# Optimization experiments

Hardware: AMD Instinct MI355X
Metric: run time of the kernel (lower is better)

## Reference

```python
import jax, jax.numpy as jnp
import numpy as np

HIDDEN = 2048
N_HEADS = 16
N_KV_HEADS = 4
HEAD_DIM = HIDDEN // N_HEADS  # 128
N_GROUPS = N_HEADS // N_KV_HEADS  # 4


def rotate_half(x):
    # interleaved rotate: (-x_odd, x_even) interleaved back
    x_even = x[..., ::2]
    x_odd = x[..., 1::2]
    return jnp.stack((-x_odd, x_even), axis=-1).reshape(x.shape)


def setup_inputs() -> dict:
    key = jax.random.key(0)
    ks = jax.random.split(key, 8)
    B, S = 4, 2048
    x = jax.random.normal(ks[0], (B, S, HIDDEN), dtype=jnp.float32)
    # RoPE tables (precomputed cos/sin over max positions)
    inv_freq = 1.0 / (1000000.0 ** (np.arange(0, HEAD_DIM, 2, dtype=np.float32) / HEAD_DIM))
    t = np.arange(S, dtype=np.float32)
    freqs = np.outer(t, inv_freq)  # [S, HEAD_DIM/2]
    emb = np.repeat(freqs, 2, axis=-1)  # interleaved layout [S, HEAD_DIM]
    cos = jnp.asarray(np.cos(emb))
    sin = jnp.asarray(np.sin(emb))
    scale = 0.02
    Wq = jax.random.normal(ks[1], (HIDDEN, N_HEADS * HEAD_DIM), dtype=jnp.float32) * scale
    Wk = jax.random.normal(ks[2], (HIDDEN, N_KV_HEADS * HEAD_DIM), dtype=jnp.float32) * scale
    Wv = jax.random.normal(ks[3], (HIDDEN, N_KV_HEADS * HEAD_DIM), dtype=jnp.float32) * scale
    Wo = jax.random.normal(ks[4], (N_HEADS * HEAD_DIM, HIDDEN), dtype=jnp.float32) * scale
    return {"x": x, "cos": cos, "sin": sin, "Wq": Wq, "Wk": Wk, "Wv": Wv, "Wo": Wo}


def reference(x, cos, sin, Wq, Wk, Wv, Wo):
    B, S, D = x.shape
    q = (x @ Wq).reshape(B, S, N_HEADS, HEAD_DIM).transpose(0, 2, 1, 3)      # [B,H,S,d]
    k = (x @ Wk).reshape(B, S, N_KV_HEADS, HEAD_DIM).transpose(0, 2, 1, 3)   # [B,Hkv,S,d]
    v = (x @ Wv).reshape(B, S, N_KV_HEADS, HEAD_DIM).transpose(0, 2, 1, 3)
    # RoPE: position_ids = arange(S); cos/sin [S,d] -> [1,1,S,d]
    c = cos[:S][None, None, :, :]
    s = sin[:S][None, None, :, :]
    q = q * c + rotate_half(q) * s
    k = k * c + rotate_half(k) * s
    # repeat_kv: [B,Hkv,S,d] -> [B,H,S,d]
    k = jnp.repeat(k, N_GROUPS, axis=1)
    v = jnp.repeat(v, N_GROUPS, axis=1)
    # causal SDPA
    scores = jnp.einsum("bhqd,bhkd->bhqk", q, k) / jnp.sqrt(jnp.float32(HEAD_DIM))
    neg = jnp.finfo(scores.dtype).min
    causal = jnp.triu(jnp.full((S, S), neg, dtype=scores.dtype), k=1)
    scores = scores + causal[None, None]
    attn = jax.nn.softmax(scores.astype(jnp.float32), axis=-1).astype(q.dtype)
    out = jnp.einsum("bhqk,bhkd->bhqd", attn, v)
    out = out.transpose(0, 2, 1, 3).reshape(B, S, N_HEADS * HEAD_DIM)
    return out @ Wo
```

## Files before the change

kernel.cpp:

```cpp
#include <hip/hip_runtime.h>
#include <stdint.h>

#define S_LEN 2048
#define BATCH 4
#define HID   2048
#define HD    128
#define NKV   4
#define MTOT  (BATCH*S_LEN)
#define NQT2  (S_LEN/256)
#define QSCALE 0.08838834764831845f

typedef float    f32x4  __attribute__((ext_vector_type(4)));
typedef __bf16   bf16x8 __attribute__((ext_vector_type(8)));
typedef __bf16   bf16x4 __attribute__((ext_vector_type(4)));
typedef unsigned u32x2  __attribute__((ext_vector_type(2)));

__device__ __forceinline__ void gld16(const void* g, void* l) {
    __builtin_amdgcn_global_load_lds(
        (const __attribute__((address_space(1))) void*)g,
        (__attribute__((address_space(3))) void*)l, 16, 0, 0);
}

__global__ void k_conv_x(const float* __restrict__ in, __bf16* __restrict__ out) {
    int i = blockIdx.x * blockDim.x + threadIdx.x;
    f32x4 a = ((const f32x4*)in)[2 * i];
    f32x4 b = ((const f32x4*)in)[2 * i + 1];
    bf16x8 o;
    o[0] = (__bf16)a[0]; o[1] = (__bf16)a[1]; o[2] = (__bf16)a[2]; o[3] = (__bf16)a[3];
    o[4] = (__bf16)b[0]; o[5] = (__bf16)b[1]; o[6] = (__bf16)b[2]; o[7] = (__bf16)b[3];
    ((bf16x8*)out)[i] = o;
}

__global__ void k_transpose_all(const float* __restrict__ Wq,
                                const float* __restrict__ Wk,
                                const float* __restrict__ Wv,
                                const float* __restrict__ Wo,
                                __bf16* __restrict__ wqt,
                                __bf16* __restrict__ wkvt,
                                __bf16* __restrict__ wot) {
    const int z = blockIdx.z;
    const float* in; __bf16* out; int N;
    if      (z == 0) { in = Wq; out = wqt;  N = 2048; }
    else if (z == 1) { in = Wk; out = wkvt; N = 512;  }
    else if (z == 2) { in = Wv; out = wkvt + (size_t)512 * HID; N = 512; }
    else             { in = Wo; out = wot;  N = 2048; }
    int k0 = blockIdx.x * 64, n0 = blockIdx.y * 64;
    if (n0 >= N) return;
    __shared__ float tile[64][65];
    for (int e = threadIdx.x; e < 4096; e += 256) {
        int r = e >> 6, c = e & 63;
        tile[r][c] = in[(size_t)(k0 + r) * N + n0 + c];
    }
    __syncthreads();
    for (int e = threadIdx.x; e < 4096; e += 256) {
        int r = e >> 6, c = e & 63;
        out[(size_t)(n0 + r) * HID + k0 + c] = (__bf16)tile[c][r];
    }
}

#define BARM asm volatile("s_barrier" ::: "memory")
#define BAR1 do { BARM;                                                       \
                  asm volatile("s_waitcnt lgkmcnt(0)" ::: "memory");          \
                  __builtin_amdgcn_sched_barrier(0); } while (0)
#define BAR2 BARM
#define MM(qm, qn)                                                            \
    do {                                                                      \
        __builtin_amdgcn_s_setprio(1);                                        \
        _Pragma("unroll") for (int ks = 0; ks < 2; ks++)                      \
        _Pragma("unroll") for (int mf = 0; mf < 4; mf++)                      \
        _Pragma("unroll") for (int nf = 0; nf < 2; nf++)                      \
            acc[qm][qn][mf][nf] = __builtin_amdgcn_mfma_f32_16x16x32_bf16(    \
                af[mf][ks], bf[nf][ks], acc[qm][qn][mf][nf], 0, 0, 0);        \
        __builtin_amdgcn_s_setprio(0);                                        \
    } while (0)

#define GEMM8_BODY(Aptr, Bptr)                                                \
    __shared__ __bf16 Ab[2][2][128 * 64];                                     \
    __shared__ __bf16 Bb[2][2][128 * 64];                                     \
    const int tid = threadIdx.x, lane = tid & 63, wave = tid >> 6;            \
    const int wm = wave >> 2, wn = wave & 3;                                  \
    const int lo = lane & 15, hi = lane >> 4;                                 \
    f32x4 acc[2][2][4][2] = {};                                               \
    const int srow = wave * 8 + (lane >> 3);                                  \
    const int sp   = lane & 7;                                                \
    auto STA = [&](int s, int h, int t) {                                     \
        _Pragma("unroll") for (int p = 0; p < 2; p++) {                       \
            int rr = p * 64 + srow;                                           \
            int c = sp ^ (rr & 7);                                            \
            gld16(Aptr + (size_t)(m0 + h * 128 + rr) * HID + t * 64 + c * 8,  \
                  &Ab[s][h][(p * 64 + wave * 8) * 64]);                       \
        }                                                                     \
    };                                                                        \
    auto STB = [&](int s, int h, int t) {                                     \
        _Pragma("unroll") for (int p = 0; p < 2; p++) {                       \
            int rr = p * 64 + srow;                                           \
            int c = sp ^ (rr & 7);                                            \
            gld16(Bptr + (size_t)(n0 + h * 128 + rr) * HID + t * 64 + c * 8,  \
                  &Bb[s][h][(p * 64 + wave * 8) * 64]);                       \
        }                                                                     \
    };                                                                        \
    bf16x8 af[4][2], bf[2][2];                                                \
    auto LDA = [&](int s, int qm) {                                           \
        _Pragma("unroll") for (int mf = 0; mf < 4; mf++) {                    \
            int rr = wm * 64 + mf * 16 + lo;                                  \
            _Pragma("unroll") for (int ks = 0; ks < 2; ks++) {                \
                int pp = (ks * 4 + hi) ^ (rr & 7);                            \
                af[mf][ks] = *(const bf16x8*)&Ab[s][qm][rr * 64 + pp * 8];    \
            }                                                                 \
        }                                                                     \
    };                                                                        \
    auto LDB = [&](int s, int qn) {                                           \
        _Pragma("unroll") for (int nf = 0; nf < 2; nf++) {                    \
            int rr = wn * 32 + nf * 16 + lo;                                  \
            _Pragma("unroll") for (int ks = 0; ks < 2; ks++) {                \
                int pp = (ks * 4 + hi) ^ (rr & 7);                            \
                bf[nf][ks] = *(const bf16x8*)&Bb[s][qn][rr * 64 + pp * 8];    \
            }                                                                 \
        }                                                                     \
    };                                                                        \
    STA(0, 0, 0); STB(0, 0, 0); STA(0, 1, 0); STB(0, 1, 0);                   \
    STA(1, 1, 1); STB(1, 1, 1);                                               \
    asm volatile("s_waitcnt vmcnt(4)" ::: "memory");                          \
    BARM;                                                                     \
    _Pragma("unroll 1")                                                       \
    for (int i = 0; i < 16; i++) {                                            \
        const int t0 = 2 * i, t1 = 2 * i + 1;                                 \
        const bool more = (i < 15);                                           \
        LDA(0, 0); LDB(0, 0);                                                 \
        STA(1, 0, t1); STB(1, 0, t1);                                         \
        BAR1; MM(0, 0); BAR2;                                                 \
        LDB(0, 1);                                                            \
        BAR1; MM(0, 1); BAR2;                                                 \
        LDA(0, 1); LDB(0, 0);                                                 \
        if (more) STA(0, 0, t0 + 2);                                          \
        BAR1; MM(1, 0); BAR2;                                                 \
        LDB(0, 1);                                                            \
        if (more) STB(0, 0, t0 + 2);                                          \
        BAR1; MM(1, 1);                                                       \
        if (more) { asm volatile("s_waitcnt vmcnt(4)" ::: "memory"); }        \
        else      { asm volatile("s_waitcnt vmcnt(0)" ::: "memory"); }        \
        BAR2;                                                                 \
        LDA(1, 1); LDB(1, 1);                                                 \
        if (more) { STA(0, 1, t0 + 2); STB(0, 1, t0 + 2); }                   \
        BAR1; MM(1, 1); BAR2;                                                 \
        LDB(1, 0);                                                            \
        BAR1; MM(1, 0); BAR2;                                                 \
        LDA(1, 0); LDB(1, 1);                                                 \
        if (more) STA(1, 1, t1 + 2);                                          \
        BAR1; MM(0, 1); BAR2;                                                 \
        LDB(1, 0);                                                            \
        if (more) STB(1, 1, t1 + 2);                                          \
        BAR1; MM(0, 0);                                                       \
        if (more) { asm volatile("s_waitcnt vmcnt(4)" ::: "memory"); }        \
        BAR2;                                                                 \
    }

__global__ __launch_bounds__(512) void k_gemm_q8(const __bf16* __restrict__ A,
                                                 const __bf16* __restrict__ Bt,
                                                 unsigned char* __restrict__ qb8,
                                                 const float* __restrict__ cosp,
                                                 const float* __restrict__ sinp) {
    const int m0 = (blockIdx.x >> 3) * 256;
    const int n0 = (blockIdx.x & 7) * 256;
    GEMM8_BODY(A, Bt)

    __bf16* Cs = (__bf16*)&Ab[0][0][0];
    const int crow = tid >> 4;
    const int cch  = tid & 15;
    const int d0 = cch * 8;
#pragma unroll
    for (int qm = 0; qm < 2; qm++)
#pragma unroll
        for (int qn = 0; qn < 2; qn++) {
#pragma unroll
            for (int mf = 0; mf < 4; mf++)
#pragma unroll
                for (int nf = 0; nf < 2; nf++) {
                    int rl = wm * 64 + mf * 16 + hi * 4;
                    int cl = wn * 32 + nf * 16 + lo;
#pragma unroll
                    for (int r = 0; r < 4; r++)
                        Cs[(rl + r) * 132 + cl] = (__bf16)acc[qm][qn][mf][nf][r];
                }
            __syncthreads();
#pragma unroll
            for (int rep = 0; rep < 4; rep++) {
                int row = rep * 32 + crow;
                int rowg = m0 + qm * 128 + row;
                int colg = n0 + qn * 128 + cch * 8;
                bf16x8 v = *(const bf16x8*)&Cs[row * 132 + cch * 8];
                float f[8];
#pragma unroll
                for (int j = 0; j < 8; j++) f[j] = (float)v[j];
                int s = rowg & (S_LEN - 1);
                f32x4 c0 = *(const f32x4*)&cosp[s * HD + d0];
                f32x4 c1 = *(const f32x4*)&cosp[s * HD + d0 + 4];
                f32x4 s0 = *(const f32x4*)&sinp[s * HD + d0];
                f32x4 s1 = *(const f32x4*)&sinp[s * HD + d0 + 4];
                float cc[8] = {c0[0], c0[1], c0[2], c0[3], c1[0], c1[1], c1[2], c1[3]};
                float ss[8] = {s0[0], s0[1], s0[2], s0[3], s1[0], s1[1], s1[2], s1[3]};
#pragma unroll
                for (int p = 0; p < 4; p++) {
                    float e0 = f[2 * p], e1 = f[2 * p + 1];
                    f[2 * p]     = (e0 * cc[2 * p]     - e1 * ss[2 * p])     * QSCALE;
                    f[2 * p + 1] = (e1 * cc[2 * p + 1] + e0 * ss[2 * p + 1]) * QSCALE;
                }
                int u0 = __builtin_amdgcn_cvt_pk_fp8_f32(f[0], f[1], 0, false);
                u0     = __builtin_amdgcn_cvt_pk_fp8_f32(f[2], f[3], u0, true);
                int u1 = __builtin_amdgcn_cvt_pk_fp8_f32(f[4], f[5], 0, false);
                u1     = __builtin_amdgcn_cvt_pk_fp8_f32(f[6], f[7], u1, true);
                u32x2 pk; pk[0] = (unsigned)u0; pk[1] = (unsigned)u1;
                *(u32x2*)&qb8[(size_t)rowg * HID + colg] = pk;
            }
            __syncthreads();
        }
}

__global__ __launch_bounds__(512) void k_gemm_o8(const __bf16* __restrict__ A,
                                                 const __bf16* __restrict__ Bt,
                                                 float* __restrict__ Cp) {
    const int m0 = (blockIdx.x >> 3) * 256;
    const int n0 = (blockIdx.x & 7) * 256;
    GEMM8_BODY(A, Bt)

#pragma unroll
    for (int qm = 0; qm < 2; qm++)
#pragma unroll
        for (int qn = 0; qn < 2; qn++)
#pragma unroll
            for (int mf = 0; mf < 4; mf++)
#pragma unroll
                for (int nf = 0; nf < 2; nf++) {
                    int row = m0 + qm * 128 + wm * 64 + mf * 16 + hi * 4;
                    int col = n0 + qn * 128 + wn * 32 + nf * 16 + lo;
#pragma unroll
                    for (int r = 0; r < 4; r++)
                        Cp[(size_t)(row + r) * HID + col] = acc[qm][qn][mf][nf][r];
                }
}

__global__ __launch_bounds__(256) void k_gemm_kv(const __bf16* __restrict__ A,
                                                 const __bf16* __restrict__ Bt,
                                                 unsigned char* __restrict__ kb8,
                                                 __bf16* __restrict__ vtb,
                                                 const float* __restrict__ cosp,
                                                 const float* __restrict__ sinp) {
    __shared__ __align__(16) char smem[33792];
    __bf16* As = (__bf16*)smem;
    __bf16* Bs = (__bf16*)(smem + 16384);
    const int tid = threadIdx.x, lane = tid & 63, wave = tid >> 6;
    const int wm = wave >> 1, wn = wave & 1;
    const int m0 = blockIdx.x * 128;
    const int n0 = 2048 + blockIdx.y * 128;
    const int lo = lane & 15, hi = lane >> 4;
    f32x4 acc[4][4] = {};

    const int srow = wave * 8 + (lane >> 3);
    const int sp   = lane & 7;

    for (int kt = 0; kt < HID; kt += 64) {
#pragma unroll
        for (int r = 0; r < 4; r++) {
            int row = r * 32 + srow;
            int c = sp ^ (row & 7);
            gld16(A + (size_t)(m0 + row) * HID + kt + c * 8, &As[(r * 32 + wave * 8) * 64]);
        }
#pragma unroll
        for (int r = 0; r < 4; r++) {
            int row = r * 32 + srow;
            int c = sp ^ (row & 7);
            gld16(Bt + (size_t)(n0 + row) * HID + kt + c * 8, &Bs[(r * 32 + wave * 8) * 64]);
        }
        __syncthreads();
#pragma unroll
        for (int ks = 0; ks < 2; ks++) {
            bf16x8 af[4], bfr[4];
#pragma unroll
            for (int mt = 0; mt < 4; mt++) {
                int row = wm * 64 + mt * 16 + lo;
                int pp = (ks * 4 + hi) ^ (row & 7);
                af[mt] = *(const bf16x8*)&As[row * 64 + pp * 8];
            }
#pragma unroll
            for (int nt = 0; nt < 4; nt++) {
                int row = wn * 64 + nt * 16 + lo;
                int pp = (ks * 4 + hi) ^ (row & 7);
                bfr[nt] = *(const bf16x8*)&Bs[row * 64 + pp * 8];
            }
#pragma unroll
            for (int mt = 0; mt < 4; mt++)
#pragma unroll
                for (int nt = 0; nt < 4; nt++)
                    acc[mt][nt] = __builtin_amdgcn_mfma_f32_16x16x32_bf16(
                        af[mt], bfr[nt], acc[mt][nt], 0, 0, 0);
        }
        __syncthreads();
    }

    if (n0 < 2560) {
        __bf16* Cs = (__bf16*)smem;
#pragma unroll
        for (int mt = 0; mt < 4; mt++)
#pragma unroll
            for (int nt = 0; nt < 4; nt++) {
                int rl = wm * 64 + mt * 16 + hi * 4;
                int cl = wn * 64 + nt * 16 + lo;
#pragma unroll
                for (int r = 0; r < 4; r++)
                    Cs[(rl + r) * 132 + cl] = (__bf16)acc[mt][nt][r];
            }
        __syncthreads();

        const int crow = tid >> 4;
        const int cch  = tid & 15;
        const int colg = n0 + cch * 8;
        const int d0 = colg & (HD - 1);
#pragma unroll
        for (int rep = 0; rep < 8; rep++) {
            int row = rep * 16 + crow;
            int rowg = m0 + row;
            bf16x8 v = *(const bf16x8*)&Cs[row * 132 + cch * 8];
            float f[8];
#pragma unroll
            for (int j = 0; j < 8; j++) f[j] = (float)v[j];
            int s = rowg & (S_LEN - 1);
            f32x4 c0 = *(const f32x4*)&cosp[s * HD + d0];
            f32x4 c1 = *(const f32x4*)&cosp[s * HD + d0 + 4];
            f32x4 s0 = *(const f32x4*)&sinp[s * HD + d0];
            f32x4 s1 = *(const f32x4*)&sinp[s * HD + d0 + 4];
            float cc[8] = {c0[0], c0[1], c0[2], c0[3], c1[0], c1[1], c1[2], c1[3]};
            float ss[8] = {s0[0], s0[1], s0[2], s0[3], s1[0], s1[1], s1[2], s1[3]};
#pragma unroll
            for (int p = 0; p < 4; p++) {
                float e0 = f[2 * p], e1 = f[2 * p + 1];
                f[2 * p]     = e0 * cc[2 * p]     - e1 * ss[2 * p];
                f[2 * p + 1] = e1 * cc[2 * p + 1] + e0 * ss[2 * p + 1];
            }
            int u0 = __builtin_amdgcn_cvt_pk_fp8_f32(f[0], f[1], 0, false);
            u0     = __builtin_amdgcn_cvt_pk_fp8_f32(f[2], f[3], u0, true);
            int u1 = __builtin_amdgcn_cvt_pk_fp8_f32(f[4], f[5], 0, false);
            u1     = __builtin_amdgcn_cvt_pk_fp8_f32(f[6], f[7], u1, true);
            u32x2 pk; pk[0] = (unsigned)u0; pk[1] = (unsigned)u1;
            *(u32x2*)&kb8[(size_t)rowg * 512 + (colg - 2048)] = pk;
        }
    } else {
        __bf16* CsT = (__bf16*)smem;
#pragma unroll
        for (int mt = 0; mt < 4; mt++)
#pragma unroll
            for (int nt = 0; nt < 4; nt++) {
                int cl = wn * 64 + nt * 16 + lo;
                int mrow = wm * 64 + mt * 16 + hi * 4;
                bf16x4 w;
#pragma unroll
                for (int r = 0; r < 4; r++) w[r] = (__bf16)acc[mt][nt][r];
                *(bf16x4*)&CsT[cl * 132 + mrow] = w;
            }
        __syncthreads();

        const int kvh = (n0 - 2560) >> 7;
        const int bb = m0 >> 11;
        const int s0 = m0 & (S_LEN - 1);
        __bf16* dst = vtb + (size_t)(bb * NKV + kvh) * HD * S_LEN;
        const int dloc = tid >> 4;
        const int sch  = tid & 15;
#pragma unroll
        for (int rep = 0; rep < 8; rep++) {
            int d = rep * 16 + dloc;
            bf16x8 v = *(const bf16x8*)&CsT[d * 132 + sch * 8];
            *(bf16x8*)&dst[(size_t)d * S_LEN + s0 + sch * 8] = v;
        }
    }
}

__global__ __launch_bounds__(512) void k_attn(const unsigned char* __restrict__ qb8,
                                              const unsigned char* __restrict__ kb8,
                                              const __bf16* __restrict__ vtb,
                                              __bf16* __restrict__ ob) {
    __shared__ char   Ks8[2][64 * 128];
    __shared__ __bf16 Vs[2][128 * 64];
    __shared__ __bf16 Ps[8][2048];
    const int tid = threadIdx.x, lane = tid & 63, wave = tid >> 6;
    const int pair = blockIdx.x, h = blockIdx.y, b = blockIdx.z;
    const int kvh = h >> 2;
    const int lo = lane & 15, hi = lane >> 4;
    char* PsW = (char*)&Ps[wave][0];

    const unsigned char* kbb = kb8 + (size_t)b * S_LEN * 512 + kvh * HD;
    const __bf16* vbb = vtb + (size_t)(b * NKV + kvh) * HD * S_LEN;

    const int krow_s = tid >> 3;
    const int kp_s   = tid & 7;
    const int vrow_s = wave * 8 + (lane >> 3);
    const int vp_s   = lane & 7;

    auto STAGE_K = [&](int buf, int t) {
        int c = kp_s ^ (krow_s & 7);
        gld16(kbb + (size_t)(t * 64 + krow_s) * 512 + c * 16,
              &Ks8[buf][wave * 1024]);
    };
    auto STAGE_V = [&](int buf, int t) {
#pragma unroll
        for (int r = 0; r < 2; r++) {
            int row = r * 64 + vrow_s;
            int c = vp_s ^ (row & 7);
            gld16(vbb + (size_t)row * S_LEN + t * 64 + c * 8,
                  &Vs[buf][(r * 64 + wave * 8) * 64]);
        }
    };

    auto SM = [&](f32x4 (&sc)[4], float& Mr, float& Lr, f32x4 (&o)[8]) {
        float mloc = sc[0][0];
#pragma unroll
        for (int nt = 0; nt < 4; nt++)
#pragma unroll
            for (int r = 0; r < 4; r++) mloc = fmaxf(mloc, sc[nt][r]);
        mloc = fmaxf(mloc, __shfl_xor(mloc, 16, 64));
        mloc = fmaxf(mloc, __shfl_xor(mloc, 32, 64));
        float mn = (mloc <= Mr + 8.f) ? Mr : mloc;
        float sum = 0.f;
#pragma unroll
        for (int nt = 0; nt < 4; nt++)
#pragma unroll
            for (int r = 0; r < 4; r++) {
                float e = __expf(sc[nt][r] - mn);
                sc[nt][r] = e;
                sum += e;
            }
        sum += __shfl_xor(sum, 16, 64);
        sum += __shfl_xor(sum, 32, 64);
        if (mn != Mr) {
            float scl = __expf(Mr - mn);
            Lr = Lr * scl + sum;
            Mr = mn;
#pragma unroll
            for (int dt = 0; dt < 8; dt++) o[dt] *= scl;
        } else {
            Lr += sum;
        }
    };

#pragma unroll 1
    for (int pi = 0; pi < 2; pi++) {
        const int qt = pi ? (NQT2 - 1 - pair) : pair;
        const int nkv = 4 * qt + 4;
        const int qbase = qt * 256 + wave * 32;

        const unsigned char* qp0 = qb8 + (size_t)(b * S_LEN + qbase + lo) * HID + h * HD;
        const unsigned char* qp1 = qp0 + (size_t)16 * HID;
        long qa0[4], qa1[4];
#pragma unroll
        for (int kf = 0; kf < 4; kf++) {
            qa0[kf] = *(const long*)(qp0 + kf * 32 + hi * 8);
            qa1[kf] = *(const long*)(qp1 + kf * 32 + hi * 8);
        }

        f32x4 o0[8] = {}, o1[8] = {};
        float Mr0 = -3e30f, Lr0 = 0.f, Mr1 = -3e30f, Lr1 = 0.f;

        int cur = 0;
        if (pi == 1) __syncthreads();
        STAGE_K(0, 0);
        STAGE_V(0, 0);
        __syncthreads();

#pragma unroll 1
        for (int t = 0; t < nkv; t++) {
            if (t < nkv - 1) { STAGE_K(cur ^ 1, t + 1); STAGE_V(cur ^ 1, t + 1); }

            f32x4 sc0[4], sc1[4];
            __builtin_amdgcn_s_setprio(1);
#pragma unroll
            for (int nt = 0; nt < 4; nt++) {
                f32x4 a = {0.f, 0.f, 0.f, 0.f}, bb = {0.f, 0.f, 0.f, 0.f};
#pragma unroll
                for (int kf = 0; kf < 4; kf++) {
                    int row = nt * 16 + lo;
                    int lch = 2 * kf + (hi >> 1);
                    long kf8 = *(const long*)&Ks8[cur][row * 128 +
                                ((lch ^ (row & 7)) * 16) + (hi & 1) * 8];
                    a  = __builtin_amdgcn_mfma_f32_16x16x32_fp8_fp8(kf8, qa0[kf], a, 0, 0, 0);
                    bb = __builtin_amdgcn_mfma_f32_16x16x32_fp8_fp8(kf8, qa1[kf], bb, 0, 0, 0);
                }
                sc0[nt] = a; sc1[nt] = bb;
            }
            __builtin_amdgcn_s_setprio(0);

            if (t * 64 + 63 > qbase) {
                int qg = qbase + lo;
#pragma unroll
                for (int nt = 0; nt < 4; nt++)
#pragma unroll
                    for (int r = 0; r < 4; r++) {
                        int kg = t * 64 + nt * 16 + hi * 4 + r;
                        if (kg > qg) sc0[nt][r] = -1e30f;
                    }
            }
            if (t * 64 + 63 > qbase + 16) {
                int qg = qbase + 16 + lo;
#pragma unroll
                for (int nt = 0; nt < 4; nt++)
#pragma unroll
                    for (int r = 0; r < 4; r++) {
                        int kg = t * 64 + nt * 16 + hi * 4 + r;
                        if (kg > qg) sc1[nt][r] = -1e30f;
                    }
            }

            SM(sc0, Mr0, Lr0, o0);
            SM(sc1, Mr1, Lr1, o1);

#pragma unroll
            for (int nt = 0; nt < 4; nt++) {
                bf16x4 p0, p1;
#pragma unroll
                for (int r = 0; r < 4; r++) { p0[r] = (__bf16)sc0[nt][r]; p1[r] = (__bf16)sc1[nt][r]; }
                int off = lo * 128 + ((nt * 32 + hi * 8) ^ ((lo & 7) << 4));
                *(bf16x4*)(PsW + off)        = p0;
                *(bf16x4*)(PsW + 2048 + off) = p1;
            }
            asm volatile("s_waitcnt lgkmcnt(0)" ::: "memory");
            bf16x8 pf0[2], pf1[2];
#pragma unroll
            for (int c = 0; c < 2; c++) {
                int off = lo * 128 + ((c * 64 + hi * 16) ^ ((lo & 7) << 4));
                pf0[c] = *(const bf16x8*)(PsW + off);
                pf1[c] = *(const bf16x8*)(PsW + 2048 + off);
            }
            __builtin_amdgcn_s_setprio(1);
#pragma unroll
            for (int dt = 0; dt < 8; dt++) {
                int rowd = dt * 16 + lo;
#pragma unroll
                for (int c = 0; c < 2; c++) {
                    int ch = c * 4 + hi;
                    bf16x8 vv = *(const bf16x8*)&Vs[cur][rowd * 64 + (ch ^ (rowd & 7)) * 8];
                    o0[dt] = __builtin_amdgcn_mfma_f32_16x16x32_bf16(vv, pf0[c], o0[dt], 0, 0, 0);
                    o1[dt] = __builtin_amdgcn_mfma_f32_16x16x32_bf16(vv, pf1[c], o1[dt], 0, 0, 0);
                }
            }
            __builtin_amdgcn_s_setprio(0);
            __syncthreads();
            cur ^= 1;
        }

        const int qe = lane >> 2, c4 = lane & 3;
#pragma unroll
        for (int sub = 0; sub < 2; sub++) {
            float rl = 1.0f / (sub ? Lr1 : Lr0);
            char* Pp = PsW + sub * 2048;
#pragma unroll
            for (int h2 = 0; h2 < 2; h2++) {
#pragma unroll
                for (int dt4 = 0; dt4 < 4; dt4++) {
                    f32x4 ov = sub ? o1[h2 * 4 + dt4] : o0[h2 * 4 + dt4];
                    bf16x4 w;
#pragma unroll
                    for (int r = 0; r < 4; r++) w[r] = (__bf16)(ov[r] * rl);
                    *(bf16x4*)(Pp + lo * 128 + ((dt4 * 32 + hi * 8) ^ ((lo & 7) << 4))) = w;
                }
                asm volatile("s_waitcnt lgkmcnt(0)" ::: "memory");
                __builtin_amdgcn_sched_barrier(0);
#pragma unroll
                for (int s2 = 0; s2 < 2; s2++) {
                    int ch = c4 + s2 * 4;
                    bf16x8 v = *(const bf16x8*)(Pp + qe * 128 + ((ch * 16) ^ ((qe & 7) << 4)));
                    int qg = qbase + sub * 16 + qe;
                    int col = h * HD + h2 * 64 + ch * 8;
                    *(bf16x8*)&ob[(size_t)(b * S_LEN + qg) * HID + col] = v;
                }
            }
        }
    }
}

extern "C" void kernel_launch(void* const* d_in, const int* in_sizes, int n_in,
                              void* d_out, int out_size, void* d_ws, size_t ws_size,
                              hipStream_t stream) {
    (void)in_sizes; (void)n_in; (void)out_size; (void)ws_size;
    const float* x    = (const float*)d_in[0];
    const float* cosp = (const float*)d_in[1];
    const float* sinp = (const float*)d_in[2];
    const float* Wq   = (const float*)d_in[3];
    const float* Wk   = (const float*)d_in[4];
    const float* Wv   = (const float*)d_in[5];
    const float* Wo   = (const float*)d_in[6];
    float* out = (float*)d_out;

    char* ws = (char*)d_ws;
    __bf16*        xb   = (__bf16*)(ws);
    __bf16*        wqt  = (__bf16*)(ws + 33554432);
    __bf16*        wkvt = (__bf16*)(ws + 41943040);
    __bf16*        wot  = (__bf16*)(ws + 46137344);
    unsigned char* qb8  = (unsigned char*)(ws + 54525952);
    unsigned char* kb8  = (unsigned char*)(ws + 71303168);
    __bf16*        vtb  = (__bf16*)(ws + 75497472);
    __bf16*        aob  = xb;

    k_conv_x<<<MTOT * HID / 8 / 256, 256, 0, stream>>>(x, xb);
    { dim3 g(32, 32, 4);
      k_transpose_all<<<g, 256, 0, stream>>>(Wq, Wk, Wv, Wo, wqt, wkvt, wot); }

    k_gemm_q8<<<256, 512, 0, stream>>>(xb, wqt, qb8, cosp, sinp);
    { dim3 g(64, 8); k_gemm_kv<<<g, 256, 0, stream>>>(xb, wqt, kb8, vtb, cosp, sinp); }

    { dim3 g(NQT2 / 2, 16, BATCH); k_attn<<<g, 512, 0, stream>>>(qb8, kb8, vtb, aob); }

    k_gemm_o8<<<256, 512, 0, stream>>>(aob, wot, out);
}
```

Before: 319.2 us.

## Double attention KV tile to 128 and fold log2e into Q for exp2

The attention kernel now stages 128 keys and values per iteration instead of 64. This halves the number of loop iterations, barriers and softmax rescale steps, and the P·V product is processed in two 64-key halves through the per-wave P buffer. Separately, log2(e) is folded into the Q scale during the Q projection epilogue, so the softmax can use the native exp2 instruction instead of __expf. The cost is doubled LDS for K and V, which may lower occupancy, and more score registers per thread.

Result: faster. 300.3 us (-5.9%).

```diff
diff --git a/kernel.cpp b/kernel.cpp
--- a/kernel.cpp
+++ b/kernel.cpp
@@ -9,6 +9,9 @@
 #define MTOT  (BATCH*S_LEN)
 #define NQT2  (S_LEN/256)
 #define QSCALE 0.08838834764831845f
+#define LOG2E  1.4426950408889634f
+
+#define EXP2F(x) __builtin_amdgcn_exp2f(x)
 
 typedef float    f32x4  __attribute__((ext_vector_type(4)));
 typedef __bf16   bf16x8 __attribute__((ext_vector_type(8)));
@@ -168,6 +171,7 @@
     const int crow = tid >> 4;
     const int cch  = tid & 15;
     const int d0 = cch * 8;
+    const float QS2 = QSCALE * LOG2E;
 #pragma unroll
     for (int qm = 0; qm < 2; qm++)
 #pragma unroll
@@ -202,8 +206,8 @@
 #pragma unroll
                 for (int p = 0; p < 4; p++) {
                     float e0 = f[2 * p], e1 = f[2 * p + 1];
-                    f[2 * p]     = (e0 * cc[2 * p]     - e1 * ss[2 * p])     * QSCALE;
-                    f[2 * p + 1] = (e1 * cc[2 * p + 1] + e0 * ss[2 * p + 1]) * QSCALE;
+                    f[2 * p]     = (e0 * cc[2 * p]     - e1 * ss[2 * p])     * QS2;
+                    f[2 * p + 1] = (e1 * cc[2 * p + 1] + e0 * ss[2 * p + 1]) * QS2;
                 }
                 int u0 = __builtin_amdgcn_cvt_pk_fp8_f32(f[0], f[1], 0, false);
                 u0     = __builtin_amdgcn_cvt_pk_fp8_f32(f[2], f[3], u0, true);
@@ -377,8 +381,8 @@
                                               const unsigned char* __restrict__ kb8,
                                               const __bf16* __restrict__ vtb,
                                               __bf16* __restrict__ ob) {
-    __shared__ char   Ks8[2][64 * 128];
-    __shared__ __bf16 Vs[2][128 * 64];
+    __shared__ char   Ks8[2][128 * 128];
+    __shared__ __bf16 Vs[2][128 * 128];
     __shared__ __bf16 Ps[8][2048];
     const int tid = threadIdx.x, lane = tid & 63, wave = tid >> 6;
     const int pair = blockIdx.x, h = blockIdx.y, b = blockIdx.z;
@@ -391,28 +395,32 @@
 
     const int krow_s = tid >> 3;
     const int kp_s   = tid & 7;
-    const int vrow_s = wave * 8 + (lane >> 3);
-    const int vp_s   = lane & 7;
+    const int vrow_s = tid >> 4;
+    const int vp_s   = tid & 15;
 
     auto STAGE_K = [&](int buf, int t) {
-        int c = kp_s ^ (krow_s & 7);
-        gld16(kbb + (size_t)(t * 64 + krow_s) * 512 + c * 16,
-              &Ks8[buf][wave * 1024]);
+#pragma unroll
+        for (int r = 0; r < 2; r++) {
+            int row = r * 64 + krow_s;
+            int c = kp_s ^ (row & 7);
+            gld16(kbb + (size_t)(t * 128 + row) * 512 + c * 16,
+                  &Ks8[buf][(r * 64 + wave * 8) * 128]);
+        }
     };
     auto STAGE_V = [&](int buf, int t) {
 #pragma unroll
-        for (int r = 0; r < 2; r++) {
-            int row = r * 64 + vrow_s;
-            int c = vp_s ^ (row & 7);
-            gld16(vbb + (size_t)row * S_LEN + t * 64 + c * 8,
-                  &Vs[buf][(r * 64 + wave * 8) * 64]);
+        for (int r = 0; r < 4; r++) {
+            int row = r * 32 + vrow_s;
+            int c = vp_s ^ (row & 15);
+            gld16(vbb + (size_t)row * S_LEN + t * 128 + c * 8,
+                  &Vs[buf][(r * 32 + wave * 4) * 128]);
         }
     };
 
-    auto SM = [&](f32x4 (&sc)[4], float& Mr, float& Lr, f32x4 (&o)[8]) {
+    auto SM = [&](f32x4 (&sc)[8], float& Mr, float& Lr, f32x4 (&o)[8]) {
         float mloc = sc[0][0];
 #pragma unroll
-        for (int nt = 0; nt < 4; nt++)
+        for (int nt = 0; nt < 8; nt++)
 #pragma unroll
             for (int r = 0; r < 4; r++) mloc = fmaxf(mloc, sc[nt][r]);
         mloc = fmaxf(mloc, __shfl_xor(mloc, 16, 64));
@@ -420,17 +428,17 @@
         float mn = (mloc <= Mr + 8.f) ? Mr : mloc;
         float sum = 0.f;
 #pragma unroll
-        for (int nt = 0; nt < 4; nt++)
+        for (int nt = 0; nt < 8; nt++)
 #pragma unroll
             for (int r = 0; r < 4; r++) {
-                float e = __expf(sc[nt][r] - mn);
+                float e = EXP2F(sc[nt][r] - mn);
                 sc[nt][r] = e;
                 sum += e;
             }
         sum += __shfl_xor(sum, 16, 64);
         sum += __shfl_xor(sum, 32, 64);
         if (mn != Mr) {
-            float scl = __expf(Mr - mn);
+            float scl = EXP2F(Mr - mn);
             Lr = Lr * scl + sum;
             Mr = mn;
 #pragma unroll
@@ -443,7 +451,7 @@
 #pragma unroll 1
     for (int pi = 0; pi < 2; pi++) {
         const int qt = pi ? (NQT2 - 1 - pair) : pair;
-        const int nkv = 4 * qt + 4;
+        const int nkv = 2 * qt + 2;
         const int qbase = qt * 256 + wave * 32;
 
         const unsigned char* qp0 = qb8 + (size_t)(b * S_LEN + qbase + lo) * HID + h * HD;
@@ -468,10 +476,10 @@
         for (int t = 0; t < nkv; t++) {
             if (t < nkv - 1) { STAGE_K(cur ^ 1, t + 1); STAGE_V(cur ^ 1, t + 1); }
 
-            f32x4 sc0[4], sc1[4];
+            f32x4 sc0[8], sc1[8];
             __builtin_amdgcn_s_setprio(1);
 #pragma unroll
-            for (int nt = 0; nt < 4; nt++) {
+            for (int nt = 0; nt < 8; nt++) {
                 f32x4 a = {0.f, 0.f, 0.f, 0.f}, bb = {0.f, 0.f, 0.f, 0.f};
 #pragma unroll
                 for (int kf = 0; kf < 4; kf++) {
@@ -486,23 +494,23 @@
             }
             __builtin_amdgcn_s_setprio(0);
 
-            if (t * 64 + 63 > qbase) {
+            if (t * 128 + 127 > qbase) {
                 int qg = qbase + lo;
 #pragma unroll
-                for (int nt = 0; nt < 4; nt++)
+                for (int nt = 0; nt < 8; nt++)
 #pragma unroll
                     for (int r = 0; r < 4; r++) {
-                        int kg = t * 64 + nt * 16 + hi * 4 + r;
+                        int kg = t * 128 + nt * 16 + hi * 4 + r;
                         if (kg > qg) sc0[nt][r] = -1e30f;
                     }
             }
-            if (t * 64 + 63 > qbase + 16) {
+            if (t * 128 + 127 > qbase + 16) {
                 int qg = qbase + 16 + lo;
 #pragma unroll
-                for (int nt = 0; nt < 4; nt++)
+                for (int nt = 0; nt < 8; nt++)
 #pragma unroll
                     for (int r = 0; r < 4; r++) {
-                        int kg = t * 64 + nt * 16 + hi * 4 + r;
+                        int kg = t * 128 + nt * 16 + hi * 4 + r;
                         if (kg > qg) sc1[nt][r] = -1e30f;
                     }
             }
@@ -511,35 +519,42 @@
             SM(sc1, Mr1, Lr1, o1);
 
 #pragma unroll
-            for (int nt = 0; nt < 4; nt++) {
-                bf16x4 p0, p1;
-#pragma unroll
-                for (int r = 0; r < 4; r++) { p0[r] = (__bf16)sc0[nt][r]; p1[r] = (__bf16)sc1[nt][r]; }
-                int off = lo * 128 + ((nt * 32 + hi * 8) ^ ((lo & 7) << 4));
-                *(bf16x4*)(PsW + off)        = p0;
-                *(bf16x4*)(PsW + 2048 + off) = p1;
-            }
-            asm volatile("s_waitcnt lgkmcnt(0)" ::: "memory");
-            bf16x8 pf0[2], pf1[2];
-#pragma unroll
-            for (int c = 0; c < 2; c++) {
-                int off = lo * 128 + ((c * 64 + hi * 16) ^ ((lo & 7) << 4));
-                pf0[c] = *(const bf16x8*)(PsW + off);
-                pf1[c] = *(const bf16x8*)(PsW + 2048 + off);
-            }
-            __builtin_amdgcn_s_setprio(1);
-#pragma unroll
-            for (int dt = 0; dt < 8; dt++) {
-                int rowd = dt * 16 + lo;
+            for (int hh = 0; hh < 2; hh++) {
+#pragma unroll
+                for (int ntl = 0; ntl < 4; ntl++) {
+                    int nt = hh * 4 + ntl;
+                    bf16x4 p0, p1;
+#pragma unroll
+                    for (int r = 0; r < 4; r++) { p0[r] = (__bf16)sc0[nt][r]; p1[r] = (__bf16)sc1[nt][r]; }
+                    int off = lo * 128 + ((ntl * 32 + hi * 8) ^ ((lo & 7) << 4));
+                    *(bf16x4*)(PsW + off)        = p0;
+                    *(bf16x4*)(PsW + 2048 + off) = p1;
+                }
+                asm volatile("s_waitcnt lgkmcnt(0)" ::: "memory");
+                bf16x8 pf0[2], pf1[2];
 #pragma unroll
                 for (int c = 0; c < 2; c++) {
-                    int ch = c * 4 + hi;
-                    bf16x8 vv = *(const bf16x8*)&Vs[cur][rowd * 64 + (ch ^ (rowd & 7)) * 8];
-                    o0[dt] = __builtin_amdgcn_mfma_f32_16x16x32_bf16(vv, pf0[c], o0[dt], 0, 0, 0);
-                    o1[dt] = __builtin_amdgcn_mfma_f32_16x16x32_bf16(vv, pf1[c], o1[dt], 0, 0, 0);
-                }
-            }
-            __builtin_amdgcn_s_setprio(0);
+                    int off = lo * 128 + ((c * 64 + hi * 16) ^ ((lo & 7) << 4));
+                    pf0[c] = *(const bf16x8*)(PsW + off);
+                    pf1[c] = *(const bf16x8*)(PsW + 2048 + off);
+                }
+                asm volatile("s_waitcnt lgkmcnt(0)" ::: "memory");
+                __builtin_amdgcn_sched_barrier(0);
+                __builtin_amdgcn_s_setprio(1);
+#pragma unroll
+                for (int dt = 0; dt < 8; dt++) {
+                    int rowd = dt * 16 + lo;
+#pragma unroll
+                    for (int c = 0; c < 2; c++) {
+                        int gch = hh * 8 + c * 4 + hi;
+                        bf16x8 vv = *(const bf16x8*)&Vs[cur][rowd * 128 +
+                                     (gch ^ (rowd & 15)) * 8];
+                        o0[dt] = __builtin_amdgcn_mfma_f32_16x16x32_bf16(vv, pf0[c], o0[dt], 0, 0, 0);
+                        o1[dt] = __builtin_amdgcn_mfma_f32_16x16x32_bf16(vv, pf1[c], o1[dt], 0, 0, 0);
+                    }
+                }
+                __builtin_amdgcn_s_setprio(0);
+            }
             __syncthreads();
             cur ^= 1;
         }
```
